# Kernel tuning notes

Hardware: AMD Instinct MI355X
Metric: run time of the kernel (lower is better)

## Reference

```python
import jax, jax.numpy as jnp
import numpy as np

FEAT = 36          # 4 + node_embedding_dim(32)
N_NODES = 24       # max_num_nodes_per_route
N_ROUTES = 48      # max_num_route
CUST_H = 128
CUST_OUT = 32
RNN_H = 128        # route_output_dim
B = 512


def _xavier(key, shape):
    fan_in, fan_out = shape[0], shape[1]
    lim = float(np.sqrt(6.0 / (fan_in + fan_out)))
    return jax.random.uniform(key, shape, jnp.float32, -lim, lim)


def setup_inputs() -> dict:
    key = jax.random.key(0)
    ks = jax.random.split(key, 24)
    inp = {
        "candidates": jax.random.normal(ks[0], (B, 2 * FEAT), jnp.float32),
        "customers": jax.random.normal(ks[1], (B, N_ROUTES, N_NODES * FEAT), jnp.float32),
        # Customer_Model MLP: 36 -> 128 (tanh) -> 32 (tanh)
        "cust_w1": _xavier(ks[2], (FEAT, CUST_H)),
        "cust_b1": jnp.zeros((CUST_H,), jnp.float32),
        "cust_w2": _xavier(ks[3], (CUST_H, CUST_OUT)),
        "cust_b2": jnp.zeros((CUST_OUT,), jnp.float32),
        # GRU layer 0 (input 32 -> hidden 128), gates order (r,z,n)
        "gru_wih0": _xavier(ks[4], (CUST_OUT, 3 * RNN_H)),
        "gru_whh0": _xavier(ks[5], (RNN_H, 3 * RNN_H)),
        "gru_bih0": jnp.zeros((3 * RNN_H,), jnp.float32),
        "gru_bhh0": jnp.zeros((3 * RNN_H,), jnp.float32),
        # GRU layer 1 (128 -> 128)
        "gru_wih1": _xavier(ks[6], (RNN_H, 3 * RNN_H)),
        "gru_whh1": _xavier(ks[7], (RNN_H, 3 * RNN_H)),
        "gru_bih1": jnp.zeros((3 * RNN_H,), jnp.float32),
        "gru_bhh1": jnp.zeros((3 * RNN_H,), jnp.float32),
        # candidate head and final MLP
        "cand_w": _xavier(ks[8], (2 * FEAT, 64)),
        "cand_b": jnp.zeros((64,), jnp.float32),
        "fc1_w": _xavier(ks[9], (RNN_H + 64, 128)),
        "fc1_b": jnp.zeros((128,), jnp.float32),
        "fc2_w": _xavier(ks[10], (128, 128)),
        "fc2_b": jnp.zeros((128,), jnp.float32),
        "fc3_w": _xavier(ks[11], (128, 1)),
        "fc3_b": jnp.zeros((1,), jnp.float32),
    }
    return inp


def _gru_layer(x_seq, wih, whh, bih, bhh):
    # x_seq: [T, N, in_dim]; returns [T, N, RNN_H]
    gi = jnp.einsum('tni,ih->tnh', x_seq, wih) + bih  # precompute input gates

    def step(h, gi_t):
        gh = h @ whh + bhh
        i_r, i_z, i_n = jnp.split(gi_t, 3, axis=-1)
        h_r, h_z, h_n = jnp.split(gh, 3, axis=-1)
        r = jax.nn.sigmoid(i_r + h_r)
        z = jax.nn.sigmoid(i_z + h_z)
        n = jnp.tanh(i_n + r * h_n)
        h_new = (1.0 - z) * n + z * h
        return h_new, h_new

    h0 = jnp.zeros((x_seq.shape[1], RNN_H), x_seq.dtype)
    _, out = jax.lax.scan(step, h0, gi)
    return out


def reference(candidates, customers, cust_w1, cust_b1, cust_w2, cust_b2,
              gru_wih0, gru_whh0, gru_bih0, gru_bhh0,
              gru_wih1, gru_whh1, gru_bih1, gru_bhh1,
              cand_w, cand_b, fc1_w, fc1_b, fc2_w, fc2_b, fc3_w, fc3_b):
    b = candidates.shape[0]
    x_c = candidates @ cand_w + cand_b                      # [B, 64]

    # all routes processed at once: fold routes into batch dim
    x = customers.reshape(b * N_ROUTES, N_NODES, FEAT)
    x = jnp.transpose(x, (1, 0, 2))                          # [T=24, B*48, 36]
    # Customer_Model MLP (tanh hidden, tanh output)
    x = jnp.tanh(jnp.tanh(x @ cust_w1 + cust_b1) @ cust_w2 + cust_b2)  # [24, B*48, 32]

    out = _gru_layer(x, gru_wih0, gru_whh0, gru_bih0, gru_bhh0)
    out = _gru_layer(out, gru_wih1, gru_whh1, gru_bih1, gru_bhh1)
    last = out[-1].reshape(b, N_ROUTES, RNN_H)               # last timestep per route
    x_r = last.mean(axis=1)                                  # mean over 48 routes
    # dropout is identity at inference

    h = jnp.concatenate([x_r, x_c], axis=1)                  # [B, 192]
    h = jnp.tanh(h @ fc1_w + fc1_b)
    h = jnp.tanh(h @ fc2_w + fc2_b)
    return h @ fc3_w + fc3_b                                 # [B, 1]
```

## Files before the change

### kernel.cpp

```cpp
#include <hip/hip_runtime.h>
#include <stdint.h>


#define NSEQ   24576
#define TSTEPS 24
#define SEQB   16

typedef __attribute__((ext_vector_type(8))) short bf16x8;
typedef __attribute__((ext_vector_type(4))) float floatx4;

#define PK_W1    0
#define PK_W2    8192
#define PK_WIH0  12288
#define PK_WHH0  24576
#define PK_WIH1  73728
#define PK_WHH1  122880
#define PK_END   172032
#define X2_EL    172032
#define HOUT_BYTE 38092800

#define MFMA(a,b,c) c = __builtin_amdgcn_mfma_f32_16x16x32_bf16(a, b, c, 0, 0, 0)

__device__ __forceinline__ uint16_t f2bf(float f) {
  uint32_t u = __float_as_uint(f);
  u += 0x7FFFu + ((u >> 16) & 1u);
  return (uint16_t)(u >> 16);
}
__device__ __forceinline__ uint32_t cvt_pk(float a, float b) {
  uint32_t r;
  asm("v_cvt_pk_bf16_f32 %0, %1, %2" : "=v"(r) : "v"(a), "v"(b));
  return r;
}
__device__ __forceinline__ float fast_sigmoid(float x) {
  float e = __builtin_amdgcn_exp2f(-1.4426950408889634f * x);
  return __builtin_amdgcn_rcpf(1.0f + e);
}
__device__ __forceinline__ float fast_tanh(float x) {
  float e = __builtin_amdgcn_exp2f(-2.8853900817779268f * x);
  return 2.0f * __builtin_amdgcn_rcpf(1.0f + e) - 1.0f;
}
__device__ __forceinline__ bf16x8 ldf(const uint16_t* p) {
  return *(const bf16x8*)p;
}

__global__ __launch_bounds__(256) void pack_weights(
    const float* __restrict__ w1, const float* __restrict__ w2,
    const float* __restrict__ wih0, const float* __restrict__ whh0,
    const float* __restrict__ wih1, const float* __restrict__ whh1,
    uint16_t* __restrict__ ws) {
  int idx = blockIdx.x * 256 + threadIdx.x;
  if (idx >= PK_END) return;
  const float* W; int N, KB, Kreal, base;
  if      (idx <  8192) { W = w1;   N = 128; KB = 2; Kreal = 36;  base = 0; }
  else if (idx < 12288) { W = w2;   N = 32;  KB = 4; Kreal = 128; base = 8192; }
  else if (idx < 24576) { W = wih0; N = 384; KB = 1; Kreal = 32;  base = 12288; }
  else if (idx < 73728) { W = whh0; N = 384; KB = 4; Kreal = 128; base = 24576; }
  else if (idx < 122880){ W = wih1; N = 384; KB = 4; Kreal = 128; base = 73728; }
  else                  { W = whh1; N = 384; KB = 4; Kreal = 128; base = 122880; }
  int li = idx - base;
  int frag = li >> 9;
  int e = li & 511;
  int lane = e >> 3, j = e & 7;
  int kb = frag % KB, nt = frag / KB;
  int k = kb * 32 + (lane >> 4) * 8 + j;
  int n = nt * 16 + (lane & 15);
  float v = (k < Kreal) ? W[k * N + n] : 0.0f;
  ws[base + li] = f2bf(v);
}

__global__ __launch_bounds__(256) void mlp_kernel(
    const float* __restrict__ customers, const float* __restrict__ b1,
    const float* __restrict__ b2, const uint16_t* __restrict__ wpk,
    uint16_t* __restrict__ x2out) {
  __shared__ uint16_t sA[128 * 136];
  const int r0 = blockIdx.x * 128;
  const int t  = r0 / NSEQ;
  const int s0 = r0 % NSEQ;
  const int tid = threadIdx.x;
  const int w = tid >> 6, l = tid & 63, q = l >> 4, c = l & 15;
  const int lo8 = l * 8;
  const int hb = 4 * q;

  floatx4 acc[2][8];
  #pragma unroll
  for (int mi = 0; mi < 2; ++mi)
    #pragma unroll
    for (int nt = 0; nt < 8; ++nt) acc[mi][nt] = (floatx4){0.f, 0.f, 0.f, 0.f};

  #pragma unroll
  for (int mi = 0; mi < 2; ++mi) {
    const int mt = 2 * w + mi;
    const int seq = s0 + mt * 16 + c;
    const float* xp = customers + (size_t)seq * 864 + t * 36;
    floatx4 u0 = *(const floatx4*)(xp + q * 8);
    floatx4 u1 = *(const floatx4*)(xp + q * 8 + 4);
    bf16x8 a0;
    { uint32_t* a0u = (uint32_t*)&a0;
      a0u[0] = cvt_pk(u0[0], u0[1]); a0u[1] = cvt_pk(u0[2], u0[3]);
      a0u[2] = cvt_pk(u1[0], u1[1]); a0u[3] = cvt_pk(u1[2], u1[3]); }
    bf16x8 a1x = (bf16x8){0,0,0,0,0,0,0,0};
    if (q == 0) {
      floatx4 u2 = *(const floatx4*)(xp + 32);
      uint32_t* a1u = (uint32_t*)&a1x;
      a1u[0] = cvt_pk(u2[0], u2[1]); a1u[1] = cvt_pk(u2[2], u2[3]);
    }
    #pragma unroll
    for (int nt = 0; nt < 8; ++nt) {
      bf16x8 bv0 = ldf(wpk + PK_W1 + (nt * 2 + 0) * 512 + lo8);
      bf16x8 bv1 = ldf(wpk + PK_W1 + (nt * 2 + 1) * 512 + lo8);
      MFMA(bv0, a0,  acc[mi][nt]);
      MFMA(bv1, a1x, acc[mi][nt]);
    }
  }
  #pragma unroll
  for (int mi = 0; mi < 2; ++mi) {
    const int mt = 2 * w + mi;
    #pragma unroll
    for (int nt = 0; nt < 8; ++nt) {
      const floatx4 bv = *(const floatx4*)(b1 + nt * 16 + hb);
      float o0 = fast_tanh(acc[mi][nt][0] + bv[0]);
      float o1 = fast_tanh(acc[mi][nt][1] + bv[1]);
      float o2 = fast_tanh(acc[mi][nt][2] + bv[2]);
      float o3 = fast_tanh(acc[mi][nt][3] + bv[3]);
      uint2 pk; pk.x = cvt_pk(o0, o1); pk.y = cvt_pk(o2, o3);
      *(uint2*)&sA[(mt * 16 + c) * 136 + nt * 16 + hb] = pk;
    }
  }
  __syncthreads();

  floatx4 acc2[2][2];
  #pragma unroll
  for (int mi = 0; mi < 2; ++mi)
    #pragma unroll
    for (int nt = 0; nt < 2; ++nt) acc2[mi][nt] = (floatx4){0.f, 0.f, 0.f, 0.f};

  #pragma unroll
  for (int kb = 0; kb < 4; ++kb) {
    bf16x8 av0 = ldf(&sA[((2 * w + 0) * 16 + c) * 136 + kb * 32 + q * 8]);
    bf16x8 av1 = ldf(&sA[((2 * w + 1) * 16 + c) * 136 + kb * 32 + q * 8]);
    #pragma unroll
    for (int nt = 0; nt < 2; ++nt) {
      bf16x8 bv = ldf(wpk + PK_W2 + (nt * 4 + kb) * 512 + lo8);
      MFMA(bv, av0, acc2[0][nt]);
      MFMA(bv, av1, acc2[1][nt]);
    }
  }
  #pragma unroll
  for (int mi = 0; mi < 2; ++mi) {
    const int mt = 2 * w + mi;
    #pragma unroll
    for (int nt = 0; nt < 2; ++nt) {
      const floatx4 bv = *(const floatx4*)(b2 + nt * 16 + hb);
      float o0 = fast_tanh(acc2[mi][nt][0] + bv[0]);
      float o1 = fast_tanh(acc2[mi][nt][1] + bv[1]);
      float o2 = fast_tanh(acc2[mi][nt][2] + bv[2]);
      float o3 = fast_tanh(acc2[mi][nt][3] + bv[3]);
      uint2 pk; pk.x = cvt_pk(o0, o1); pk.y = cvt_pk(o2, o3);
      *(uint2*)(x2out + (size_t)(r0 + mt * 16 + c) * 32 + nt * 16 + hb) = pk;
    }
  }
}

__global__ __launch_bounds__(512, 2) void gru_res(
    const uint16_t* __restrict__ wpk, const uint16_t* __restrict__ x2,
    const float* __restrict__ bih0, const float* __restrict__ bhh0,
    const float* __restrict__ bih1, const float* __restrict__ bhh1,
    float* __restrict__ hout) {
  __shared__ uint16_t h0l[2][SEQB * 136];
  __shared__ uint16_t h1l[2][SEQB * 136];
  __shared__ float bias_l[8][128];
  const int seq0 = blockIdx.x * SEQB;
  const int tid = threadIdx.x;
  const int J = tid >> 6, l = tid & 63, q = l >> 4, c = l & 15;
  const int lo8 = l * 8;

  for (int i = tid; i < 1088; i += 512) ((uint32_t*)h1l[0])[i] = 0u;
  for (int i = tid; i < 1024; i += 512) {
    int g = i >> 7, k = i & 127;
    float v;
    if      (g == 0) v = bih0[k]       + bhh0[k];
    else if (g == 1) v = bih0[128 + k] + bhh0[128 + k];
    else if (g == 2) v = bih0[256 + k];
    else if (g == 3) v = bhh0[256 + k];
    else if (g == 4) v = bih1[k]       + bhh1[k];
    else if (g == 5) v = bih1[128 + k] + bhh1[128 + k];
    else if (g == 6) v = bih1[256 + k];
    else             v = bhh1[256 + k];
    bias_l[g][k] = v;
  }

  bf16x8 wi0[3], wh0[3][4], wi1[3][4], wh1[3][4];
  #pragma unroll
  for (int g = 0; g < 3; ++g) {
    wi0[g] = ldf(wpk + PK_WIH0 + (g * 8 + J) * 512 + lo8);
    #pragma unroll
    for (int kb = 0; kb < 4; ++kb) {
      wh0[g][kb] = ldf(wpk + PK_WHH0 + ((g * 8 + J) * 4 + kb) * 512 + lo8);
      wi1[g][kb] = ldf(wpk + PK_WIH1 + ((g * 8 + J) * 4 + kb) * 512 + lo8);
      wh1[g][kb] = ldf(wpk + PK_WHH1 + ((g * 8 + J) * 4 + kb) * 512 + lo8);
    }
  }
  const int hb = J * 16 + 4 * q;

  floatx4 h0m, h1m = (floatx4){0.f, 0.f, 0.f, 0.f};

  bf16x8 ax0 = ldf(x2 + (size_t)(seq0 + c) * 32 + q * 8);
  bf16x8 ax  = ldf(x2 + ((size_t)NSEQ + seq0 + c) * 32 + q * 8);
  __syncthreads();

  {
    floatx4 aR = *(const floatx4*)&bias_l[0][hb];
    floatx4 aZ = *(const floatx4*)&bias_l[1][hb];
    floatx4 aN = *(const floatx4*)&bias_l[2][hb];
    floatx4 aH = *(const floatx4*)&bias_l[3][hb];
    MFMA(wi0[0], ax0, aR); MFMA(wi0[1], ax0, aZ); MFMA(wi0[2], ax0, aN);
    float o[4];
    #pragma unroll
    for (int e = 0; e < 4; ++e) {
      float r  = fast_sigmoid(aR[e]);
      float zz = fast_sigmoid(aZ[e]);
      float nn = fast_tanh(aN[e] + r * aH[e]);
      o[e] = nn - zz * nn;
      h0m[e] = o[e];
    }
    uint2 pk; pk.x = cvt_pk(o[0], o[1]); pk.y = cvt_pk(o[2], o[3]);
    *(uint2*)(h0l[0] + c * 136 + hb) = pk;
  }
  __syncthreads();

  #pragma unroll 1
  for (int t = 0; t < TSTEPS; ++t) {
    const uint16_t* h0cur = h0l[t & 1];
    const uint16_t* h1prv = h1l[t & 1];
    uint16_t* h0nxt = h0l[(t + 1) & 1];
    uint16_t* h1cur = h1l[(t + 1) & 1];
    const int tnx = (t + 2 < TSTEPS) ? t + 2 : TSTEPS - 1;
    bf16x8 axn = ldf(x2 + ((size_t)tnx * NSEQ + seq0 + c) * 32 + q * 8);

    floatx4 aR1 = *(const floatx4*)&bias_l[4][hb];
    floatx4 aZ1 = *(const floatx4*)&bias_l[5][hb];
    floatx4 aN1 = *(const floatx4*)&bias_l[6][hb];
    floatx4 aH1 = *(const floatx4*)&bias_l[7][hb];
    floatx4 aR0 = *(const floatx4*)&bias_l[0][hb];
    floatx4 aZ0 = *(const floatx4*)&bias_l[1][hb];
    floatx4 aN0 = *(const floatx4*)&bias_l[2][hb];
    floatx4 aH0 = *(const floatx4*)&bias_l[3][hb];

    #pragma unroll
    for (int kb = 0; kb < 4; ++kb) {
      bf16x8 a0 = ldf(h0cur + c * 136 + kb * 32 + q * 8);
      bf16x8 ah = ldf(h1prv + c * 136 + kb * 32 + q * 8);
      MFMA(wi1[0][kb], a0, aR1); MFMA(wh1[0][kb], ah, aR1);
      MFMA(wi1[1][kb], a0, aZ1); MFMA(wh1[1][kb], ah, aZ1);
      MFMA(wi1[2][kb], a0, aN1); MFMA(wh1[2][kb], ah, aH1);
      MFMA(wh0[0][kb], a0, aR0);
      MFMA(wh0[1][kb], a0, aZ0);
      MFMA(wh0[2][kb], a0, aH0);
    }
    MFMA(wi0[0], ax, aR0); MFMA(wi0[1], ax, aZ0); MFMA(wi0[2], ax, aN0);

    {
      float o[4];
      #pragma unroll
      for (int e = 0; e < 4; ++e) {
        float r  = fast_sigmoid(aR1[e]);
        float zz = fast_sigmoid(aZ1[e]);
        float nn = fast_tanh(aN1[e] + r * aH1[e]);
        o[e] = nn + zz * (h1m[e] - nn);
        h1m[e] = o[e];
      }
      uint2 pk; pk.x = cvt_pk(o[0], o[1]); pk.y = cvt_pk(o[2], o[3]);
      *(uint2*)(h1cur + c * 136 + hb) = pk;
    }
    {
      float o[4];
      #pragma unroll
      for (int e = 0; e < 4; ++e) {
        float r  = fast_sigmoid(aR0[e]);
        float zz = fast_sigmoid(aZ0[e]);
        float nn = fast_tanh(aN0[e] + r * aH0[e]);
        o[e] = nn + zz * (h0m[e] - nn);
        h0m[e] = o[e];
      }
      uint2 pk; pk.x = cvt_pk(o[0], o[1]); pk.y = cvt_pk(o[2], o[3]);
      *(uint2*)(h0nxt + c * 136 + hb) = pk;
    }
    __syncthreads();
    ax = axn;
  }

  *(floatx4*)(hout + (size_t)(seq0 + c) * 128 + hb) = h1m;
}

__global__ __launch_bounds__(192) void final_kernel(
    const float* __restrict__ hout, const float* __restrict__ cands,
    const float* __restrict__ cw, const float* __restrict__ cb,
    const float* __restrict__ f1w, const float* __restrict__ f1b,
    const float* __restrict__ f2w, const float* __restrict__ f2b,
    const float* __restrict__ f3w, const float* __restrict__ f3b,
    float* __restrict__ out) {
  __shared__ float hc[192];
  __shared__ float v1[128];
  __shared__ float v2[128];
  __shared__ float red[128];
  const int b = blockIdx.x, tid = threadIdx.x;
  if (tid < 128) {
    float s = 0.f;
    const float* hp = hout + (size_t)(b * 48) * 128 + tid;
    #pragma unroll 4
    for (int r = 0; r < 48; ++r) s += hp[r * 128];
    hc[tid] = s * (1.0f / 48.0f);
  } else {
    int j = tid - 128;
    float s = cb[j];
    const float* cp = cands + b * 72;
    #pragma unroll 8
    for (int k = 0; k < 72; ++k) s += cp[k] * cw[k * 64 + j];
    hc[128 + j] = s;
  }
  __syncthreads();
  if (tid < 128) {
    float s = f1b[tid];
    for (int k = 0; k < 192; ++k) s += hc[k] * f1w[k * 128 + tid];
    v1[tid] = fast_tanh(s);
  }
  __syncthreads();
  if (tid < 128) {
    float s = f2b[tid];
    for (int k = 0; k < 128; ++k) s += v1[k] * f2w[k * 128 + tid];
    v2[tid] = fast_tanh(s);
  }
  __syncthreads();
  if (tid < 128) red[tid] = v2[tid] * f3w[tid];
  __syncthreads();
  if (tid < 64) {
    float s = red[tid] + red[tid + 64];
    s += __shfl_down(s, 32);
    s += __shfl_down(s, 16);
    s += __shfl_down(s, 8);
    s += __shfl_down(s, 4);
    s += __shfl_down(s, 2);
    s += __shfl_down(s, 1);
    if (tid == 0) out[b] = s + f3b[0];
  }
}

extern "C" void kernel_launch(void* const* d_in, const int* in_sizes, int n_in,
                              void* d_out, int out_size, void* d_ws, size_t ws_size,
                              hipStream_t stream) {
  const float* cand  = (const float*)d_in[0];
  const float* cust  = (const float*)d_in[1];
  const float* w1    = (const float*)d_in[2];
  const float* b1    = (const float*)d_in[3];
  const float* w2    = (const float*)d_in[4];
  const float* b2    = (const float*)d_in[5];
  const float* wih0  = (const float*)d_in[6];
  const float* whh0  = (const float*)d_in[7];
  const float* bih0  = (const float*)d_in[8];
  const float* bhh0  = (const float*)d_in[9];
  const float* wih1  = (const float*)d_in[10];
  const float* whh1  = (const float*)d_in[11];
  const float* bih1  = (const float*)d_in[12];
  const float* bhh1  = (const float*)d_in[13];
  const float* cw    = (const float*)d_in[14];
  const float* cb    = (const float*)d_in[15];
  const float* f1w   = (const float*)d_in[16];
  const float* f1b   = (const float*)d_in[17];
  const float* f2w   = (const float*)d_in[18];
  const float* f2b   = (const float*)d_in[19];
  const float* f3w   = (const float*)d_in[20];
  const float* f3b   = (const float*)d_in[21];

  uint16_t* wsp = (uint16_t*)d_ws;
  uint16_t* x2p = wsp + X2_EL;
  float* hout = (float*)((char*)d_ws + HOUT_BYTE);
  float* outp = (float*)d_out;

  pack_weights<<<(PK_END + 255) / 256, 256, 0, stream>>>(w1, w2, wih0, whh0, wih1, whh1, wsp);
  mlp_kernel<<<(NSEQ * TSTEPS) / 128, 256, 0, stream>>>(cust, b1, b2, wsp, x2p);
  gru_res<<<NSEQ / SEQB, 512, 0, stream>>>(wsp, x2p, bih0, bhh0, bih1, bhh1, hout);
  final_kernel<<<512, 192, 0, stream>>>(hout, cand, cw, cb, f1w, f1b, f2w, f2b, f3w, f3b, outp);
}
```

Baseline: 420.0 us.

## Process two 16-sequence tiles per GRU block to amortize register weights

Raises the per-block sequence count from 16 to 32, with each block running two MFMA tiles per timestep that share the register-resident GRU weights. This halves the number of blocks, so weight loads and __syncthreads per sequence drop, and the two independent tiles give the scheduler more work to hide latency. In exchange, register pressure rises (two sets of hidden-state accumulators) and LDS doubles, which may hurt occupancy at 2 blocks per SM. The grid launch must also be sized for SEQB=32, which is assumed to be derived from the macro.

```diff
diff --git a/kernel.cpp b/kernel.cpp
--- a/kernel.cpp
+++ b/kernel.cpp
@@ -4,7 +4,7 @@
 
 #define NSEQ   24576
 #define TSTEPS 24
-#define SEQB   16
+#define SEQB   32
 
 typedef __attribute__((ext_vector_type(8))) short bf16x8;
 typedef __attribute__((ext_vector_type(4))) float floatx4;
@@ -174,7 +174,7 @@
   const int J = tid >> 6, l = tid & 63, q = l >> 4, c = l & 15;
   const int lo8 = l * 8;
 
-  for (int i = tid; i < 1088; i += 512) ((uint32_t*)h1l[0])[i] = 0u;
+  for (int i = tid; i < 2176; i += 512) ((uint32_t*)h1l[0])[i] = 0u;
   for (int i = tid; i < 1024; i += 512) {
     int g = i >> 7, k = i & 127;
     float v;
@@ -202,31 +202,89 @@
   }
   const int hb = J * 16 + 4 * q;
 
-  floatx4 h0m, h1m = (floatx4){0.f, 0.f, 0.f, 0.f};
-
-  bf16x8 ax0 = ldf(x2 + (size_t)(seq0 + c) * 32 + q * 8);
-  bf16x8 ax  = ldf(x2 + ((size_t)NSEQ + seq0 + c) * 32 + q * 8);
-  __syncthreads();
-
-  {
-    floatx4 aR = *(const floatx4*)&bias_l[0][hb];
-    floatx4 aZ = *(const floatx4*)&bias_l[1][hb];
-    floatx4 aN = *(const floatx4*)&bias_l[2][hb];
-    floatx4 aH = *(const floatx4*)&bias_l[3][hb];
-    MFMA(wi0[0], ax0, aR); MFMA(wi0[1], ax0, aZ); MFMA(wi0[2], ax0, aN);
-    float o[4];
-    #pragma unroll
-    for (int e = 0; e < 4; ++e) {
-      float r  = fast_sigmoid(aR[e]);
-      float zz = fast_sigmoid(aZ[e]);
-      float nn = fast_tanh(aN[e] + r * aH[e]);
-      o[e] = nn - zz * nn;
-      h0m[e] = o[e];
-    }
-    uint2 pk; pk.x = cvt_pk(o[0], o[1]); pk.y = cvt_pk(o[2], o[3]);
-    *(uint2*)(h0l[0] + c * 136 + hb) = pk;
-  }
-  __syncthreads();
+  floatx4 h0m0 = (floatx4){0.f,0.f,0.f,0.f}, h0m1 = (floatx4){0.f,0.f,0.f,0.f};
+  floatx4 h1m0 = (floatx4){0.f,0.f,0.f,0.f}, h1m1 = (floatx4){0.f,0.f,0.f,0.f};
+
+  bf16x8 ax_0 = ldf(x2 + (size_t)(seq0 + c) * 32 + q * 8);
+  bf16x8 ax_1 = ldf(x2 + (size_t)(seq0 + 16 + c) * 32 + q * 8);
+  __syncthreads();
+
+  #define GRU_PRO(TI, AX, H0M)                                              \
+  {                                                                         \
+    floatx4 aR = *(const floatx4*)&bias_l[0][hb];                           \
+    floatx4 aZ = *(const floatx4*)&bias_l[1][hb];                           \
+    floatx4 aN = *(const floatx4*)&bias_l[2][hb];                           \
+    floatx4 aH = *(const floatx4*)&bias_l[3][hb];                           \
+    MFMA(wi0[0], AX, aR); MFMA(wi0[1], AX, aZ); MFMA(wi0[2], AX, aN);       \
+    float o[4];                                                             \
+    _Pragma("unroll")                                                       \
+    for (int e = 0; e < 4; ++e) {                                           \
+      float r  = fast_sigmoid(aR[e]);                                       \
+      float zz = fast_sigmoid(aZ[e]);                                       \
+      float nn = fast_tanh(aN[e] + r * aH[e]);                              \
+      o[e] = nn - zz * nn;                                                  \
+      H0M[e] = o[e];                                                        \
+    }                                                                       \
+    uint2 pk; pk.x = cvt_pk(o[0], o[1]); pk.y = cvt_pk(o[2], o[3]);         \
+    *(uint2*)(h0l[0] + ((TI) * 16 + c) * 136 + hb) = pk;                    \
+  }
+  GRU_PRO(0, ax_0, h0m0)
+  GRU_PRO(1, ax_1, h0m1)
+  #undef GRU_PRO
+  __syncthreads();
+
+  ax_0 = ldf(x2 + ((size_t)NSEQ + seq0 + c) * 32 + q * 8);
+  ax_1 = ldf(x2 + ((size_t)NSEQ + seq0 + 16 + c) * 32 + q * 8);
+
+  #define GRU_TILE(TI, AX, H0M, H1M)                                        \
+  {                                                                         \
+    floatx4 aR1 = *(const floatx4*)&bias_l[4][hb];                          \
+    floatx4 aZ1 = *(const floatx4*)&bias_l[5][hb];                          \
+    floatx4 aN1 = *(const floatx4*)&bias_l[6][hb];                          \
+    floatx4 aH1 = *(const floatx4*)&bias_l[7][hb];                          \
+    floatx4 aR0 = *(const floatx4*)&bias_l[0][hb];                          \
+    floatx4 aZ0 = *(const floatx4*)&bias_l[1][hb];                          \
+    floatx4 aN0 = *(const floatx4*)&bias_l[2][hb];                          \
+    floatx4 aH0 = *(const floatx4*)&bias_l[3][hb];                          \
+    _Pragma("unroll")                                                       \
+    for (int kb = 0; kb < 4; ++kb) {                                        \
+      bf16x8 a0 = ldf(h0cur + ((TI) * 16 + c) * 136 + kb * 32 + q * 8);     \
+      bf16x8 ah = ldf(h1prv + ((TI) * 16 + c) * 136 + kb * 32 + q * 8);     \
+      MFMA(wi1[0][kb], a0, aR1); MFMA(wh1[0][kb], ah, aR1);                 \
+      MFMA(wi1[1][kb], a0, aZ1); MFMA(wh1[1][kb], ah, aZ1);                 \
+      MFMA(wi1[2][kb], a0, aN1); MFMA(wh1[2][kb], ah, aH1);                 \
+      MFMA(wh0[0][kb], a0, aR0);                                            \
+      MFMA(wh0[1][kb], a0, aZ0);                                            \
+      MFMA(wh0[2][kb], a0, aH0);                                            \
+    }                                                                       \
+    MFMA(wi0[0], AX, aR0); MFMA(wi0[1], AX, aZ0); MFMA(wi0[2], AX, aN0);    \
+    {                                             \
+      float o[4];                                                           \
+      _Pragma("unroll")                                                     \
+      for (int e = 0; e < 4; ++e) {                                         \
+        float r  = fast_sigmoid(aR1[e]);                                    \
+        float zz = fast_sigmoid(aZ1[e]);                                    \
+        float nn = fast_tanh(aN1[e] + r * aH1[e]);                          \
+        o[e] = nn + zz * (H1M[e] - nn);                                     \
+        H1M[e] = o[e];                                                      \
+      }                                                                     \
+      uint2 pk; pk.x = cvt_pk(o[0], o[1]); pk.y = cvt_pk(o[2], o[3]);       \
+      *(uint2*)(h1cur + ((TI) * 16 + c) * 136 + hb) = pk;                   \
+    }                                                                       \
+    {                                           \
+      float o[4];                                                           \
+      _Pragma("unroll")                                                     \
+      for (int e = 0; e < 4; ++e) {                                         \
+        float r  = fast_sigmoid(aR0[e]);                                    \
+        float zz = fast_sigmoid(aZ0[e]);                                    \
+        float nn = fast_tanh(aN0[e] + r * aH0[e]);                          \
+        o[e] = nn + zz * (H0M[e] - nn);                                     \
+        H0M[e] = o[e];                                                      \
+      }                                                                     \
+      uint2 pk; pk.x = cvt_pk(o[0], o[1]); pk.y = cvt_pk(o[2], o[3]);       \
+      *(uint2*)(h0nxt + ((TI) * 16 + c) * 136 + hb) = pk;                   \
+    }                                                                       \
+  }
 
   #pragma unroll 1
   for (int t = 0; t < TSTEPS; ++t) {
@@ -235,61 +293,20 @@
     uint16_t* h0nxt = h0l[(t + 1) & 1];
     uint16_t* h1cur = h1l[(t + 1) & 1];
     const int tnx = (t + 2 < TSTEPS) ? t + 2 : TSTEPS - 1;
-    bf16x8 axn = ldf(x2 + ((size_t)tnx * NSEQ + seq0 + c) * 32 + q * 8);
-
-    floatx4 aR1 = *(const floatx4*)&bias_l[4][hb];
-    floatx4 aZ1 = *(const floatx4*)&bias_l[5][hb];
-    floatx4 aN1 = *(const floatx4*)&bias_l[6][hb];
-    floatx4 aH1 = *(const floatx4*)&bias_l[7][hb];
-    floatx4 aR0 = *(const floatx4*)&bias_l[0][hb];
-    floatx4 aZ0 = *(const floatx4*)&bias_l[1][hb];
-    floatx4 aN0 = *(const floatx4*)&bias_l[2][hb];
-    floatx4 aH0 = *(const floatx4*)&bias_l[3][hb];
-
-    #pragma unroll
-    for (int kb = 0; kb < 4; ++kb) {
-      bf16x8 a0 = ldf(h0cur + c * 136 + kb * 32 + q * 8);
-      bf16x8 ah = ldf(h1prv + c * 136 + kb * 32 + q * 8);
-      MFMA(wi1[0][kb], a0, aR1); MFMA(wh1[0][kb], ah, aR1);
-      MFMA(wi1[1][kb], a0, aZ1); MFMA(wh1[1][kb], ah, aZ1);
-      MFMA(wi1[2][kb], a0, aN1); MFMA(wh1[2][kb], ah, aH1);
-      MFMA(wh0[0][kb], a0, aR0);
-      MFMA(wh0[1][kb], a0, aZ0);
-      MFMA(wh0[2][kb], a0, aH0);
-    }
-    MFMA(wi0[0], ax, aR0); MFMA(wi0[1], ax, aZ0); MFMA(wi0[2], ax, aN0);
-
-    {
-      float o[4];
-      #pragma unroll
-      for (int e = 0; e < 4; ++e) {
-        float r  = fast_sigmoid(aR1[e]);
-        float zz = fast_sigmoid(aZ1[e]);
-        float nn = fast_tanh(aN1[e] + r * aH1[e]);
-        o[e] = nn + zz * (h1m[e] - nn);
-        h1m[e] = o[e];
-      }
-      uint2 pk; pk.x = cvt_pk(o[0], o[1]); pk.y = cvt_pk(o[2], o[3]);
-      *(uint2*)(h1cur + c * 136 + hb) = pk;
-    }
-    {
-      float o[4];
-      #pragma unroll
-      for (int e = 0; e < 4; ++e) {
-        float r  = fast_sigmoid(aR0[e]);
-        float zz = fast_sigmoid(aZ0[e]);
-        float nn = fast_tanh(aN0[e] + r * aH0[e]);
-        o[e] = nn + zz * (h0m[e] - nn);
-        h0m[e] = o[e];
-      }
-      uint2 pk; pk.x = cvt_pk(o[0], o[1]); pk.y = cvt_pk(o[2], o[3]);
-      *(uint2*)(h0nxt + c * 136 + hb) = pk;
-    }
+    bf16x8 axn_0 = ldf(x2 + ((size_t)tnx * NSEQ + seq0 + c) * 32 + q * 8);
+    bf16x8 axn_1 = ldf(x2 + ((size_t)tnx * NSEQ + seq0 + 16 + c) * 32 + q * 8);
+
+    GRU_TILE(0, ax_0, h0m0, h1m0)
+    __builtin_amdgcn_sched_barrier(0);
+    GRU_TILE(1, ax_1, h0m1, h1m1)
+
     __syncthreads();
-    ax = axn;
-  }
-
-  *(floatx4*)(hout + (size_t)(seq0 + c) * 128 + hb) = h1m;
+    ax_0 = axn_0; ax_1 = axn_1;
+  }
+  #undef GRU_TILE
+
+  *(floatx4*)(hout + (size_t)(seq0 + c) * 128 + hb) = h1m0;
+  *(floatx4*)(hout + (size_t)(seq0 + 16 + c) * 128 + hb) = h1m1;
 }
 
 __global__ __launch_bounds__(192) void final_kernel(
```

Result: faster. 411.7 us (-2.0%).

## Process two 16-sequence tiles per GRU block and merge sigmoid reciprocals

Applied to the files above, without the earlier changes.

Each gru_res block now handles 32 sequences as two 16-row MFMA tiles that share the register-resident weights, halving the block count and the per-sequence barrier and weight-load overhead. Gate math moves into a helper that computes both sigmoids with one reciprocal of the product of their denominators. The x prefetch distance drops from two steps ahead to one, and LDS use for the hidden-state buffers doubles. Register pressure rises with twice the accumulators, which may hurt occupancy under launch_bounds(512,2). The product-of-denominators trick can overflow for large negative gate inputs.

```diff
diff --git a/kernel.cpp b/kernel.cpp
--- a/kernel.cpp
+++ b/kernel.cpp
@@ -4,7 +4,7 @@
 
 #define NSEQ   24576
 #define TSTEPS 24
-#define SEQB   16
+#define SEQB   32
 
 typedef __attribute__((ext_vector_type(8))) short bf16x8;
 typedef __attribute__((ext_vector_type(4))) float floatx4;
@@ -41,6 +41,25 @@
 }
 __device__ __forceinline__ bf16x8 ldf(const uint16_t* p) {
   return *(const bf16x8*)p;
+}
+__device__ __forceinline__ floatx4 gru_gate(floatx4 gR, floatx4 gZ,
+                                            floatx4 gN, floatx4 gH,
+                                            floatx4 hprev) {
+  floatx4 o;
+  #pragma unroll
+  for (int e = 0; e < 4; ++e) {
+    float er = __builtin_amdgcn_exp2f(-1.4426950408889634f * gR[e]);
+    float ez = __builtin_amdgcn_exp2f(-1.4426950408889634f * gZ[e]);
+    float A = 1.0f + er, B = 1.0f + ez;
+    float inv = __builtin_amdgcn_rcpf(A * B);
+    float r = B * inv;
+    float z = A * inv;
+    float m = gN[e] + r * gH[e];
+    float em = __builtin_amdgcn_exp2f(-2.8853900817779268f * m);
+    float nn = 2.0f * __builtin_amdgcn_rcpf(1.0f + em) - 1.0f;
+    o[e] = nn + z * (hprev[e] - nn);
+  }
+  return o;
 }
 
 __global__ __launch_bounds__(256) void pack_weights(
@@ -174,7 +193,7 @@
   const int J = tid >> 6, l = tid & 63, q = l >> 4, c = l & 15;
   const int lo8 = l * 8;
 
-  for (int i = tid; i < 1088; i += 512) ((uint32_t*)h1l[0])[i] = 0u;
+  for (int i = tid; i < 2176; i += 512) ((uint32_t*)h1l[0])[i] = 0u;
   for (int i = tid; i < 1024; i += 512) {
     int g = i >> 7, k = i & 127;
     float v;
@@ -202,29 +221,30 @@
   }
   const int hb = J * 16 + 4 * q;
 
-  floatx4 h0m, h1m = (floatx4){0.f, 0.f, 0.f, 0.f};
-
-  bf16x8 ax0 = ldf(x2 + (size_t)(seq0 + c) * 32 + q * 8);
-  bf16x8 ax  = ldf(x2 + ((size_t)NSEQ + seq0 + c) * 32 + q * 8);
-  __syncthreads();
+  floatx4 h0m0 = (floatx4){0.f,0.f,0.f,0.f}, h0m1 = (floatx4){0.f,0.f,0.f,0.f};
+  floatx4 h1m0 = (floatx4){0.f,0.f,0.f,0.f}, h1m1 = (floatx4){0.f,0.f,0.f,0.f};
 
   {
+    bf16x8 ax_0 = ldf(x2 + (size_t)(seq0 + c) * 32 + q * 8);
+    bf16x8 ax_1 = ldf(x2 + (size_t)(seq0 + 16 + c) * 32 + q * 8);
+    __syncthreads();
+
     floatx4 aR = *(const floatx4*)&bias_l[0][hb];
     floatx4 aZ = *(const floatx4*)&bias_l[1][hb];
     floatx4 aN = *(const floatx4*)&bias_l[2][hb];
     floatx4 aH = *(const floatx4*)&bias_l[3][hb];
-    MFMA(wi0[0], ax0, aR); MFMA(wi0[1], ax0, aZ); MFMA(wi0[2], ax0, aN);
-    float o[4];
-    #pragma unroll
-    for (int e = 0; e < 4; ++e) {
-      float r  = fast_sigmoid(aR[e]);
-      float zz = fast_sigmoid(aZ[e]);
-      float nn = fast_tanh(aN[e] + r * aH[e]);
-      o[e] = nn - zz * nn;
-      h0m[e] = o[e];
-    }
-    uint2 pk; pk.x = cvt_pk(o[0], o[1]); pk.y = cvt_pk(o[2], o[3]);
-    *(uint2*)(h0l[0] + c * 136 + hb) = pk;
+    MFMA(wi0[0], ax_0, aR); MFMA(wi0[1], ax_0, aZ); MFMA(wi0[2], ax_0, aN);
+    floatx4 bR = *(const floatx4*)&bias_l[0][hb];
+    floatx4 bZ = *(const floatx4*)&bias_l[1][hb];
+    floatx4 bN = *(const floatx4*)&bias_l[2][hb];
+    floatx4 bH = *(const floatx4*)&bias_l[3][hb];
+    MFMA(wi0[0], ax_1, bR); MFMA(wi0[1], ax_1, bZ); MFMA(wi0[2], ax_1, bN);
+    h0m0 = gru_gate(aR, aZ, aN, aH, h0m0);
+    h0m1 = gru_gate(bR, bZ, bN, bH, h0m1);
+    { uint2 pk; pk.x = cvt_pk(h0m0[0], h0m0[1]); pk.y = cvt_pk(h0m0[2], h0m0[3]);
+      *(uint2*)(h0l[0] + c * 136 + hb) = pk; }
+    { uint2 pk; pk.x = cvt_pk(h0m1[0], h0m1[1]); pk.y = cvt_pk(h0m1[2], h0m1[3]);
+      *(uint2*)(h0l[0] + (16 + c) * 136 + hb) = pk; }
   }
   __syncthreads();
 
@@ -234,8 +254,9 @@
     const uint16_t* h1prv = h1l[t & 1];
     uint16_t* h0nxt = h0l[(t + 1) & 1];
     uint16_t* h1cur = h1l[(t + 1) & 1];
-    const int tnx = (t + 2 < TSTEPS) ? t + 2 : TSTEPS - 1;
-    bf16x8 axn = ldf(x2 + ((size_t)tnx * NSEQ + seq0 + c) * 32 + q * 8);
+    const int tn = (t + 1 < TSTEPS) ? t + 1 : t;
+    bf16x8 ax0 = ldf(x2 + ((size_t)tn * NSEQ + seq0 + c) * 32 + q * 8);
+    bf16x8 ax1 = ldf(x2 + ((size_t)tn * NSEQ + seq0 + 16 + c) * 32 + q * 8);
 
     floatx4 aR1 = *(const floatx4*)&bias_l[4][hb];
     floatx4 aZ1 = *(const floatx4*)&bias_l[5][hb];
@@ -245,7 +266,6 @@
     floatx4 aZ0 = *(const floatx4*)&bias_l[1][hb];
     floatx4 aN0 = *(const floatx4*)&bias_l[2][hb];
     floatx4 aH0 = *(const floatx4*)&bias_l[3][hb];
-
     #pragma unroll
     for (int kb = 0; kb < 4; ++kb) {
       bf16x8 a0 = ldf(h0cur + c * 136 + kb * 32 + q * 8);
@@ -257,39 +277,53 @@
       MFMA(wh0[1][kb], a0, aZ0);
       MFMA(wh0[2][kb], a0, aH0);
     }
-    MFMA(wi0[0], ax, aR0); MFMA(wi0[1], ax, aZ0); MFMA(wi0[2], ax, aN0);
-
-    {
-      float o[4];
-      #pragma unroll
-      for (int e = 0; e < 4; ++e) {
-        float r  = fast_sigmoid(aR1[e]);
-        float zz = fast_sigmoid(aZ1[e]);
-        float nn = fast_tanh(aN1[e] + r * aH1[e]);
-        o[e] = nn + zz * (h1m[e] - nn);
-        h1m[e] = o[e];
-      }
-      uint2 pk; pk.x = cvt_pk(o[0], o[1]); pk.y = cvt_pk(o[2], o[3]);
-      *(uint2*)(h1cur + c * 136 + hb) = pk;
-    }
-    {
-      float o[4];
-      #pragma unroll
-      for (int e = 0; e < 4; ++e) {
-        float r  = fast_sigmoid(aR0[e]);
-        float zz = fast_sigmoid(aZ0[e]);
-        float nn = fast_tanh(aN0[e] + r * aH0[e]);
-        o[e] = nn + zz * (h0m[e] - nn);
-        h0m[e] = o[e];
-      }
-      uint2 pk; pk.x = cvt_pk(o[0], o[1]); pk.y = cvt_pk(o[2], o[3]);
-      *(uint2*)(h0nxt + c * 136 + hb) = pk;
-    }
+    MFMA(wi0[0], ax0, aR0); MFMA(wi0[1], ax0, aZ0); MFMA(wi0[2], ax0, aN0);
+
+    floatx4 bR1 = *(const floatx4*)&bias_l[4][hb];
+    floatx4 bZ1 = *(const floatx4*)&bias_l[5][hb];
+    floatx4 bN1 = *(const floatx4*)&bias_l[6][hb];
+    floatx4 bH1 = *(const floatx4*)&bias_l[7][hb];
+    #pragma unroll
+    for (int kb = 0; kb < 4; ++kb) {
+      bf16x8 b0 = ldf(h0cur + (16 + c) * 136 + kb * 32 + q * 8);
+      bf16x8 bh = ldf(h1prv + (16 + c) * 136 + kb * 32 + q * 8);
+      MFMA(wi1[0][kb], b0, bR1); MFMA(wh1[0][kb], bh, bR1);
+      MFMA(wi1[1][kb], b0, bZ1); MFMA(wh1[1][kb], bh, bZ1);
+      MFMA(wi1[2][kb], b0, bN1); MFMA(wh1[2][kb], bh, bH1);
+    }
+
+    h1m0 = gru_gate(aR1, aZ1, aN1, aH1, h1m0);
+    { uint2 pk; pk.x = cvt_pk(h1m0[0], h1m0[1]); pk.y = cvt_pk(h1m0[2], h1m0[3]);
+      *(uint2*)(h1cur + c * 136 + hb) = pk; }
+    h0m0 = gru_gate(aR0, aZ0, aN0, aH0, h0m0);
+    { uint2 pk; pk.x = cvt_pk(h0m0[0], h0m0[1]); pk.y = cvt_pk(h0m0[2], h0m0[3]);
+      *(uint2*)(h0nxt + c * 136 + hb) = pk; }
+
+    floatx4 bR0 = *(const floatx4*)&bias_l[0][hb];
+    floatx4 bZ0 = *(const floatx4*)&bias_l[1][hb];
+    floatx4 bN0 = *(const floatx4*)&bias_l[2][hb];
+    floatx4 bH0 = *(const floatx4*)&bias_l[3][hb];
+    #pragma unroll
+    for (int kb = 0; kb < 4; ++kb) {
+      bf16x8 b0 = ldf(h0cur + (16 + c) * 136 + kb * 32 + q * 8);
+      MFMA(wh0[0][kb], b0, bR0);
+      MFMA(wh0[1][kb], b0, bZ0);
+      MFMA(wh0[2][kb], b0, bH0);
+    }
+    MFMA(wi0[0], ax1, bR0); MFMA(wi0[1], ax1, bZ0); MFMA(wi0[2], ax1, bN0);
+
+    h1m1 = gru_gate(bR1, bZ1, bN1, bH1, h1m1);
+    { uint2 pk; pk.x = cvt_pk(h1m1[0], h1m1[1]); pk.y = cvt_pk(h1m1[2], h1m1[3]);
+      *(uint2*)(h1cur + (16 + c) * 136 + hb) = pk; }
+    h0m1 = gru_gate(bR0, bZ0, bN0, bH0, h0m1);
+    { uint2 pk; pk.x = cvt_pk(h0m1[0], h0m1[1]); pk.y = cvt_pk(h0m1[2], h0m1[3]);
+      *(uint2*)(h0nxt + (16 + c) * 136 + hb) = pk; }
+
     __syncthreads();
-    ax = axn;
-  }
-
-  *(floatx4*)(hout + (size_t)(seq0 + c) * 128 + hb) = h1m;
+  }
+
+  *(floatx4*)(hout + (size_t)(seq0 + c) * 128 + hb) = h1m0;
+  *(floatx4*)(hout + (size_t)(seq0 + 16 + c) * 128 + hb) = h1m1;
 }
 
 __global__ __launch_bounds__(192) void final_kernel(
```

New measurement: 419.8 us. Within noise of the previous version (-0.0%).
